# Kernel tuning notes

Measured on AMD Instinct MI355X. Metric: run time of the kernel, lower is better.

## Reference

```python
import jax, jax.numpy as jnp
import numpy as np

H = 768            # hidden_size
IMG_H = 1024       # image_hidden_size
NH = 12            # num_heads
NKV = 1            # num_kv_heads (MQA)
HD = H // NH       # head_dim = 64
FF = 4 * H         # intermediate_size = 3072
EPS = 1e-5


def layernorm(x, g, b):
    m = jnp.mean(x, axis=-1, keepdims=True)
    v = jnp.mean(jnp.square(x - m), axis=-1, keepdims=True)
    return (x - m) * jax.lax.rsqrt(v + EPS) * g + b


def setup_inputs() -> dict:
    key = jax.random.key(0)
    ks = jax.random.split(key, 12)
    B, NQ, NIMG = 8, 256, 4096
    s = 0.02
    return {
        "hidden_states": jax.random.normal(ks[0], (B, NQ, H), jnp.float32),
        "image_features": jax.random.normal(ks[1], (B, NIMG, IMG_H), jnp.float32),
        # norm_image_pre
        "ln_img_g": jnp.ones((IMG_H,), jnp.float32),
        "ln_img_b": jnp.zeros((IMG_H,), jnp.float32),
        # image_bottleneck (bias=False)
        "W_bottle": jax.random.normal(ks[2], (IMG_H, H), jnp.float32) * s,
        # norm_hidden
        "ln_h_g": jnp.ones((H,), jnp.float32),
        "ln_h_b": jnp.zeros((H,), jnp.float32),
        # to_q
        "Wq": jax.random.normal(ks[3], (H, H), jnp.float32) * s,
        "bq": jnp.zeros((H,), jnp.float32),
        # to_kv: out = num_kv_heads * head_dim * 2
        "Wkv": jax.random.normal(ks[4], (H, 2 * NKV * HD), jnp.float32) * s,
        "bkv": jnp.zeros((2 * NKV * HD,), jnp.float32),
        # to_out
        "Wo": jax.random.normal(ks[5], (H, H), jnp.float32) * s,
        "bo": jnp.zeros((H,), jnp.float32),
        # attn_out_norm
        "ln_ao_g": jnp.ones((H,), jnp.float32),
        "ln_ao_b": jnp.zeros((H,), jnp.float32),
        # gate
        "gate_param": jnp.zeros((), jnp.float32),
        # ffn_norm
        "ln_f_g": jnp.ones((H,), jnp.float32),
        "ln_f_b": jnp.zeros((H,), jnp.float32),
        # ffn
        "W1": jax.random.normal(ks[6], (H, FF), jnp.float32) * s,
        "b1": jnp.zeros((FF,), jnp.float32),
        "W2": jax.random.normal(ks[7], (FF, H), jnp.float32) * s,
        "b2": jnp.zeros((H,), jnp.float32),
    }


def reference(hidden_states, image_features, ln_img_g, ln_img_b, W_bottle,
              ln_h_g, ln_h_b, Wq, bq, Wkv, bkv, Wo, bo, ln_ao_g, ln_ao_b,
              gate_param, ln_f_g, ln_f_b, W1, b1, W2, b2):
    B, NQ, _ = hidden_states.shape
    # image pre-norm + bottleneck
    img = layernorm(image_features, ln_img_g, ln_img_b)
    img = img @ W_bottle                                   # [B, Nimg, H]
    # query path
    q_in = layernorm(hidden_states, ln_h_g, ln_h_b)
    q = (q_in @ Wq + bq).reshape(B, NQ, NH, HD).transpose(0, 2, 1, 3)  # b h i d
    # kv path (MQA: single shared KV head)
    kv = (img @ Wkv + bkv).reshape(B, -1, 2, NKV, HD)
    k = kv[:, :, 0, 0, :]                                  # [B, Nimg, HD]
    v = kv[:, :, 1, 0, :]
    scale = 1.0 / np.sqrt(HD)
    # broadcast KV across heads instead of explicit repeat
    scores = jnp.einsum('bhid,bjd->bhij', q * scale, k)    # [B, NH, NQ, Nimg]
    attn = jax.nn.softmax(scores, axis=-1)                 # dropout is identity (eval)
    out = jnp.einsum('bhij,bjd->bhid', attn, v)
    out = out.transpose(0, 2, 1, 3).reshape(B, NQ, H)
    out = out @ Wo + bo
    out = layernorm(out, ln_ao_g, ln_ao_b)
    gate = jax.nn.sigmoid(gate_param)
    h = hidden_states + gate * out
    ffn_in = layernorm(h, ln_f_g, ln_f_b)
    ffn_out = jax.nn.gelu(ffn_in @ W1 + b1, approximate=False) @ W2 + b2
    return h + ffn_out
```

## Files before the change

### kernel.cpp

```cpp
#include <hip/hip_runtime.h>
#include <cstdint>

typedef unsigned short u16;
typedef __bf16 bf16_t;
typedef bf16_t bf16x8 __attribute__((ext_vector_type(8)));
typedef float f32x4 __attribute__((ext_vector_type(4)));

__device__ __forceinline__ float b2f(u16 v) {
  union { uint32_t u; float f; } c; c.u = ((uint32_t)v) << 16; return c.f;
}
__device__ __forceinline__ u16 f2b(float f) {
  union { float f; uint32_t u; } c; c.f = f;
  uint32_t lsb = (c.u >> 16) & 1u;
  return (u16)((c.u + 0x7fffu + lsb) >> 16);
}
__device__ __forceinline__ uint4 pack8(f32x4 a, f32x4 b) {
  union { uint4 v; u16 s[8]; } r;
  r.s[0] = f2b(a[0]); r.s[1] = f2b(a[1]); r.s[2] = f2b(a[2]); r.s[3] = f2b(a[3]);
  r.s[4] = f2b(b[0]); r.s[5] = f2b(b[1]); r.s[6] = f2b(b[2]); r.s[7] = f2b(b[3]);
  return r.v;
}
__device__ __forceinline__ void phase_barrier() {
  asm volatile("s_waitcnt lgkmcnt(0)" ::: "memory");
  __builtin_amdgcn_s_barrier();
  asm volatile("" ::: "memory");
}
__device__ __forceinline__ void vm_drain() {
  asm volatile("s_waitcnt vmcnt(0)" ::: "memory");
}
__device__ __forceinline__ void gload_lds16(const u16* g, u16* l) {
  __builtin_amdgcn_global_load_lds((const __attribute__((address_space(1))) void*)g,
                                   (__attribute__((address_space(3))) void*)l, 16, 0, 0);
}
__device__ __forceinline__ int xcd_swizzle(int lid, int nwg) {
  int q = nwg >> 3, r = nwg & 7, x = lid & 7, s = lid >> 3;
  return (x < r ? x * (q + 1) : r * (q + 1) + (x - r) * q) + s;
}

__global__ __launch_bounds__(256) void transpose_f2b(const float* __restrict__ in,
                                                     u16* __restrict__ out, int R, int C) {
  __shared__ __align__(16) u16 tile[32][33];
  int tx = threadIdx.x & 31, ty = threadIdx.x >> 5;
  int c0 = blockIdx.x * 32, r0 = blockIdx.y * 32;
#pragma unroll
  for (int i = 0; i < 4; ++i) {
    int r = r0 + ty + i * 8, c = c0 + tx;
    if (r < R && c < C) tile[ty + i * 8][tx] = f2b(in[(size_t)r * C + c]);
  }
  __syncthreads();
#pragma unroll
  for (int i = 0; i < 4; ++i) {
    int oc = c0 + ty + i * 8, orr = r0 + tx;
    if (oc < C && orr < R) out[(size_t)oc * R + orr] = tile[tx][ty + i * 8];
  }
}

__global__ __launch_bounds__(256) void prep_wg(const u16* __restrict__ WT, const float* __restrict__ g,
                                               const float* __restrict__ b, u16* __restrict__ WgT,
                                               float* __restrict__ ucol, float* __restrict__ wcol,
                                               int K) {
  int n = blockIdx.x * 4 + (threadIdx.x >> 6);
  int lane = threadIdx.x & 63;
  const u16* src = WT + (size_t)n * K;
  u16* dst = WgT + (size_t)n * K;
  float su = 0.f, sw = 0.f;
  for (int k = lane; k < K; k += 64) {
    float wc = b2f(src[k]);
    float wg = g[k] * wc;
    dst[k] = f2b(wg);
    su += wg;
    sw += b[k] * wc;
  }
#pragma unroll
  for (int off = 32; off >= 1; off >>= 1) {
    su += __shfl_xor(su, off, 64);
    sw += __shfl_xor(sw, off, 64);
  }
  if (lane == 0) { ucol[n] = su; wcol[n] = sw; }
}

__global__ __launch_bounds__(256) void hs_prep(const float* __restrict__ hs, u16* __restrict__ out,
                                               float* __restrict__ rstdg, float* __restrict__ mrstdg) {
  int row = blockIdx.x * 4 + (threadIdx.x >> 6);
  int lane = threadIdx.x & 63;
  const float* x = hs + (size_t)row * 768;
  float v[12];
#pragma unroll
  for (int it = 0; it < 3; ++it) {
    int c = (lane + it * 64) * 4;
    f32x4 d = *(const f32x4*)(x + c);
    v[it * 4 + 0] = d[0]; v[it * 4 + 1] = d[1]; v[it * 4 + 2] = d[2]; v[it * 4 + 3] = d[3];
  }
  float s = 0.f, s2 = 0.f;
#pragma unroll
  for (int i = 0; i < 12; ++i) { s += v[i]; s2 += v[i] * v[i]; }
#pragma unroll
  for (int off = 32; off >= 1; off >>= 1) {
    s += __shfl_xor(s, off, 64);
    s2 += __shfl_xor(s2, off, 64);
  }
  float inv_n = 1.0f / 768.f;
  float mean = s * inv_n;
  float var = fmaxf(s2 * inv_n - mean * mean, 0.f);
  float rstd = rsqrtf(var + 1e-5f);
  if (lane == 0) { rstdg[row] = rstd; mrstdg[row] = mean * rstd; }
#pragma unroll
  for (int it = 0; it < 3; ++it) {
    int c = (lane + it * 64) * 4;
    uint2 po;
    po.x = (uint32_t)f2b(v[it * 4 + 0]) | ((uint32_t)f2b(v[it * 4 + 1]) << 16);
    po.y = (uint32_t)f2b(v[it * 4 + 2]) | ((uint32_t)f2b(v[it * 4 + 3]) << 16);
    *(uint2*)(out + (size_t)row * 768 + c) = po;
  }
}

__global__ __launch_bounds__(256) void ln_res(const u16* __restrict__ ao, const float* __restrict__ g,
                                              const float* __restrict__ bta,
                                              const float* __restrict__ hs,
                                              const float* __restrict__ gatep,
                                              float* __restrict__ hf, u16* __restrict__ hb,
                                              float* __restrict__ rstdg, float* __restrict__ mrstdg) {
  int row = blockIdx.x * 4 + (threadIdx.x >> 6);
  int lane = threadIdx.x & 63;
  const u16* xb = ao + (size_t)row * 768;
  float v[12];
#pragma unroll
  for (int it = 0; it < 3; ++it) {
    int c = (lane + it * 64) * 4;
    uint2 d = *(const uint2*)(xb + c);
    v[it * 4 + 0] = b2f(d.x & 0xffff); v[it * 4 + 1] = b2f(d.x >> 16);
    v[it * 4 + 2] = b2f(d.y & 0xffff); v[it * 4 + 3] = b2f(d.y >> 16);
  }
  float s = 0.f, s2 = 0.f;
#pragma unroll
  for (int i = 0; i < 12; ++i) { s += v[i]; s2 += v[i] * v[i]; }
#pragma unroll
  for (int off = 32; off >= 1; off >>= 1) {
    s += __shfl_xor(s, off, 64);
    s2 += __shfl_xor(s2, off, 64);
  }
  float inv_n = 1.0f / 768.f;
  float mean = s * inv_n;
  float var = fmaxf(s2 * inv_n - mean * mean, 0.f);
  float rstd = rsqrtf(var + 1e-5f);
  float gate = 1.f / (1.f + __expf(-gatep[0]));
  float hsum = 0.f, hsum2 = 0.f;
  float o[12];
#pragma unroll
  for (int it = 0; it < 3; ++it) {
    int c = (lane + it * 64) * 4;
    const float* rr = hs + (size_t)row * 768 + c;
#pragma unroll
    for (int i = 0; i < 4; ++i) {
      float hv = rr[i] + gate * ((v[it * 4 + i] - mean) * rstd * g[c + i] + bta[c + i]);
      o[it * 4 + i] = hv;
      hsum += hv; hsum2 += hv * hv;
    }
    *(f32x4*)(hf + (size_t)row * 768 + c) = (f32x4){o[it * 4 + 0], o[it * 4 + 1], o[it * 4 + 2], o[it * 4 + 3]};
    uint2 po;
    po.x = (uint32_t)f2b(o[it * 4 + 0]) | ((uint32_t)f2b(o[it * 4 + 1]) << 16);
    po.y = (uint32_t)f2b(o[it * 4 + 2]) | ((uint32_t)f2b(o[it * 4 + 3]) << 16);
    *(uint2*)(hb + (size_t)row * 768 + c) = po;
  }
#pragma unroll
  for (int off = 32; off >= 1; off >>= 1) {
    hsum += __shfl_xor(hsum, off, 64);
    hsum2 += __shfl_xor(hsum2, off, 64);
  }
  float hm = hsum * inv_n;
  float hvar = fmaxf(hsum2 * inv_n - hm * hm, 0.f);
  float hrstd = rsqrtf(hvar + 1e-5f);
  if (lane == 0) { rstdg[row] = hrstd; mrstdg[row] = hm * hrstd; }
}

template <int SPLITK, int AMODE, int BMODE, int EPI, bool OUTF32, bool VTOUT>
__device__ __forceinline__ void gemm_body(const void* __restrict__ Av, const void* __restrict__ Bv,
                                          const float* __restrict__ bias,
                                          const float* __restrict__ rstdg,
                                          const float* __restrict__ mrstdg,
                                          const float* __restrict__ ucol,
                                          const float* __restrict__ wcol,
                                          void* __restrict__ Cv, u16* __restrict__ VTout,
                                          int M, int N, int K) {
  __shared__ __align__(16) u16 aT[2][128 * 32];
  __shared__ __align__(16) u16 bT[2][128 * 32];
  __shared__ float rstd_s[EPI == 4 ? 128 : 1];
  __shared__ float mrstd_s[EPI == 4 ? 128 : 1];
  __shared__ __align__(16) u16 vtile[VTOUT ? 64 * 136 : 1];

  int gx = gridDim.x, gy = gridDim.y;
  int nwg = gx * gy * (int)gridDim.z;
  int lid = ((int)blockIdx.z * gy + (int)blockIdx.y) * gx + (int)blockIdx.x;
  int wid = xcd_swizzle(lid, nwg);
  int bz = wid / (gx * gy);
  int rem = wid - bz * (gx * gy);
  int bx = rem / gy;
  int by = rem - bx * gy;

  int t = threadIdx.x, lane = t & 63, wave = t >> 6;
  int quad = lane >> 4, lcol = lane & 15;
  int wm = (wave >> 1) * 64, wn = (wave & 1) * 64;
  const u16* Ab = (const u16*)Av;
  const float* Af = (const float*)Av;
  const u16* Bb = (const u16*)Bv;
  const float* Bf = (const float*)Bv;
  const int kchunk = (SPLITK > 1) ? K / SPLITK : K;
  const int kstart = (SPLITK > 1) ? bz * kchunk : 0;
  int rr = t >> 1, rc = t & 1;
  float sa = 0.f, sa2 = 0.f;
  f32x4 acc[4][4];
#pragma unroll
  for (int i = 0; i < 4; ++i)
#pragma unroll
    for (int j = 0; j < 4; ++j) acc[i][j] = (f32x4){0.f, 0.f, 0.f, 0.f};

  f32x4 araw[4], braw[4];

  auto dmaA = [&](int buf, int k0) {
#pragma unroll
    for (int s2 = 0; s2 < 2; ++s2) {
      int row = (wave * 2 + s2) * 16 + (lane >> 2);
      int ch = (lane & 3) ^ (row & 3);
      gload_lds16(Ab + (size_t)(bx * 128 + row) * K + kstart + k0 + ch * 8,
                  &aT[buf][(wave * 2 + s2) * 512]);
    }
  };
  auto dmaB = [&](int buf, int k0) {
#pragma unroll
    for (int s2 = 0; s2 < 2; ++s2) {
      int row = (wave * 2 + s2) * 16 + (lane >> 2);
      int ch = (lane & 3) ^ (row & 3);
      gload_lds16(Bb + (size_t)(by * 128 + row) * K + kstart + k0 + ch * 8,
                  &bT[buf][(wave * 2 + s2) * 512]);
    }
  };
  auto regloadA = [&](int k0) {
    const f32x4* p = (const f32x4*)&Af[(size_t)(bx * 128 + rr) * K + kstart + k0 + rc * 16];
#pragma unroll
    for (int i = 0; i < 4; ++i) araw[i] = p[i];
  };
  auto regstoreA = [&](int buf) {
    if (EPI == 4) {
#pragma unroll
      for (int i = 0; i < 4; ++i)
#pragma unroll
        for (int j = 0; j < 4; ++j) { sa += araw[i][j]; sa2 += araw[i][j] * araw[i][j]; }
    }
    uint4 c0 = pack8(araw[0], araw[1]), c1 = pack8(araw[2], araw[3]);
    *(uint4*)&aT[buf][rr * 32 + (((rc * 2 + 0) ^ (rr & 3)) << 3)] = c0;
    *(uint4*)&aT[buf][rr * 32 + (((rc * 2 + 1) ^ (rr & 3)) << 3)] = c1;
  };
  auto regloadB = [&](int k0) {
    const f32x4* p = (const f32x4*)&Bf[(size_t)(by * 128 + rr) * K + kstart + k0 + rc * 16];
#pragma unroll
    for (int i = 0; i < 4; ++i) braw[i] = p[i];
  };
  auto regstoreB = [&](int buf) {
    uint4 c0 = pack8(braw[0], braw[1]), c1 = pack8(braw[2], braw[3]);
    *(uint4*)&bT[buf][rr * 32 + (((rc * 2 + 0) ^ (rr & 3)) << 3)] = c0;
    *(uint4*)&bT[buf][rr * 32 + (((rc * 2 + 1) ^ (rr & 3)) << 3)] = c1;
  };
  auto stage_load = [&](int buf, int k0) {
    if (AMODE == 1) regloadA(k0); else dmaA(buf, k0);
    if (BMODE == 1) regloadB(k0); else dmaB(buf, k0);
  };
  auto stage_store = [&](int buf) {
    if (AMODE == 1) regstoreA(buf);
    if (BMODE == 1) regstoreB(buf);
  };
  auto compute = [&](int buf) {
    bf16x8 af[4], bfr[4];
#pragma unroll
    for (int mt = 0; mt < 4; ++mt) {
      int r = wm + mt * 16 + lcol;
      af[mt] = *(const bf16x8*)&aT[buf][r * 32 + (((quad ^ (r & 3))) << 3)];
    }
#pragma unroll
    for (int nt = 0; nt < 4; ++nt) {
      int r = wn + nt * 16 + lcol;
      bfr[nt] = *(const bf16x8*)&bT[buf][r * 32 + (((quad ^ (r & 3))) << 3)];
    }
#pragma unroll
    for (int mt = 0; mt < 4; ++mt)
#pragma unroll
      for (int nt = 0; nt < 4; ++nt)
        acc[mt][nt] = __builtin_amdgcn_mfma_f32_16x16x32_bf16(af[mt], bfr[nt], acc[mt][nt], 0, 0, 0);
  };

  const int nk = kchunk >> 5;
  stage_load(0, 0);
  stage_store(0);
  vm_drain();
  phase_barrier();
  int cur = 0;
  for (int kt = 0; kt < nk; ++kt) {
    bool more = kt + 1 < nk;
    if (more) stage_load(cur ^ 1, (kt + 1) << 5);
    compute(cur);
    if (more) stage_store(cur ^ 1);
    vm_drain();
    phase_barrier();
    cur ^= 1;
  }

  if (EPI == 4) {
    float s = sa, s2 = sa2;
    s += __shfl_xor(s, 1, 64);
    s2 += __shfl_xor(s2, 1, 64);
    if ((t & 1) == 0) {
      float inv_n = 1.0f / (float)K;
      float mean = s * inv_n;
      float var = fmaxf(s2 * inv_n - mean * mean, 0.f);
      float rstd = rsqrtf(var + 1e-5f);
      rstd_s[rr] = rstd;
      mrstd_s[rr] = mean * rstd;
    }
    __syncthreads();
  }

  if (VTOUT) {
    u16* kb = (u16*)Cv;
#pragma unroll
    for (int mt = 0; mt < 4; ++mt) {
#pragma unroll
      for (int nt = 0; nt < 4; ++nt) {
#pragma unroll
        for (int r = 0; r < 4; ++r) {
          int lrow = wm + mt * 16 + quad * 4 + r;
          int row = bx * 128 + lrow;
          int col = wn + nt * 16 + lcol;
          float v = rstd_s[lrow] * acc[mt][nt][r] - mrstd_s[lrow] * ucol[col] + wcol[col] + bias[col];
          u16 hv = f2b(v);
          if (wn == 0) kb[(size_t)row * 64 + col] = hv;
          else vtile[(col - 64) * 136 + lrow] = hv;
        }
      }
    }
    __syncthreads();
    int dd = t >> 2, js = (t & 3) * 32;
    int bg = bx >> 5, j0g = (bx & 31) * 128;
    u16* dst = VTout + ((size_t)bg * 64 + dd) * 4096 + j0g + js;
#pragma unroll
    for (int i = 0; i < 4; ++i)
      *(uint4*)(dst + i * 8) = *(const uint4*)&vtile[dd * 136 + js + i * 8];
    return;
  }

  u16* Cb = (u16*)Cv;
  float* Cf = (float*)Cv;
  if (SPLITK > 1) Cf += (size_t)bz * (size_t)M * (size_t)N;
#pragma unroll
  for (int mt = 0; mt < 4; ++mt) {
#pragma unroll
    for (int nt = 0; nt < 4; ++nt) {
#pragma unroll
      for (int r = 0; r < 4; ++r) {
        int lrow = wm + mt * 16 + quad * 4 + r;
        int row = bx * 128 + lrow;
        int col = by * 128 + wn + nt * 16 + lcol;
        float v = acc[mt][nt][r];
        if (EPI == 1) v += bias[col];
        if (EPI == 3 || EPI == 5)
          v = rstdg[row] * v - mrstdg[row] * ucol[col] + wcol[col] + bias[col];
        if (EPI == 5) v = 0.5f * v * (1.f + erff(v * 0.70710678118f));
        size_t idx = (size_t)row * N + col;
        if (OUTF32) Cf[idx] = v; else Cb[idx] = f2b(v);
      }
    }
  }
}

#define GEMM_ARGS const void* Av, const void* Bv, const float* bias, const float* rstdg, \
                  const float* mrstdg, const float* ucol, const float* wcol, void* Cv,   \
                  u16* VTout, int M, int N, int K
__global__ __launch_bounds__(256) void gemm_wc(GEMM_ARGS) {
  gemm_body<1, 0, 1, 0, false, false>(Av, Bv, bias, rstdg, mrstdg, ucol, wcol, Cv, VTout, M, N, K);
}
__global__ __launch_bounds__(256) void gemm_kv(GEMM_ARGS) {
  gemm_body<1, 1, 0, 4, false, true>(Av, Bv, bias, rstdg, mrstdg, ucol, wcol, Cv, VTout, M, N, K);
}
__global__ __launch_bounds__(256) void gemm_q(GEMM_ARGS) {
  gemm_body<1, 0, 0, 3, false, false>(Av, Bv, bias, rstdg, mrstdg, ucol, wcol, Cv, VTout, M, N, K);
}
__global__ __launch_bounds__(256) void gemm_o(GEMM_ARGS) {
  gemm_body<1, 0, 0, 1, false, false>(Av, Bv, bias, rstdg, mrstdg, ucol, wcol, Cv, VTout, M, N, K);
}
__global__ __launch_bounds__(256) void gemm_w1(GEMM_ARGS) {
  gemm_body<1, 0, 0, 5, false, false>(Av, Bv, bias, rstdg, mrstdg, ucol, wcol, Cv, VTout, M, N, K);
}
__global__ __launch_bounds__(256) void gemm_w2(GEMM_ARGS) {
  gemm_body<2, 0, 0, 0, true, false>(Av, Bv, bias, rstdg, mrstdg, ucol, wcol, Cv, VTout, M, N, K);
}

__global__ __launch_bounds__(256) void w2_merge(const float* __restrict__ part,
                                                const float* __restrict__ hf,
                                                const float* __restrict__ b2,
                                                float* __restrict__ out) {
  int idx = blockIdx.x * 256 + threadIdx.x;
  f32x4 p0 = ((const f32x4*)part)[idx];
  f32x4 p1 = ((const f32x4*)part)[idx + 393216];
  f32x4 h = ((const f32x4*)hf)[idx];
  f32x4 bb = ((const f32x4*)b2)[idx % 192];
  f32x4 o;
#pragma unroll
  for (int i = 0; i < 4; ++i) o[i] = p0[i] + p1[i] + h[i] + bb[i];
  ((f32x4*)out)[idx] = o;
}

__global__ __launch_bounds__(256) void attn_kernel(const u16* __restrict__ qbuf,
                                                   const u16* __restrict__ kb,
                                                   const u16* __restrict__ VT,
                                                   float* __restrict__ Opart,
                                                   float* __restrict__ lpart) {
  __shared__ __align__(16) u16 k_lds[64 * 72];
  __shared__ __align__(16) u16 vt_lds[64 * 72];
  __shared__ __align__(16) u16 p_lds[4 * 16 * 72];
  int lid = ((int)blockIdx.z * 12 + (int)blockIdx.y) * 4 + (int)blockIdx.x;
  int wid = (lid & 7) * 96 + (lid >> 3);
  int bi = wid & 3;
  int h = (wid >> 2) % 12;
  int z = wid / 48;
  int b = z >> 1, s = z & 1;
  int t = threadIdx.x;
  int wave = t >> 6, lane = t & 63, quad = lane >> 4, lcol = lane & 15;
  int i0 = bi * 64 + wave * 16;
  const u16* qrow = qbuf + ((size_t)(b * 256 + i0 + lcol) * 768 + h * 64 + quad * 8);
  bf16x8 qf0 = *(const bf16x8*)qrow;
  bf16x8 qf1 = *(const bf16x8*)(qrow + 32);
  float l_r[4] = {0.f, 0.f, 0.f, 0.f};
  f32x4 oacc[4];
#pragma unroll
  for (int nt = 0; nt < 4; ++nt) oacc[nt] = (f32x4){0.f, 0.f, 0.f, 0.f};
  int sr = t >> 2, sc = (t & 3) * 16;
  const u16* kbase = kb + (size_t)b * 4096 * 64;
  const u16* vtbase = VT + (size_t)b * 64 * 4096;
  u16* pw = &p_lds[wave * 16 * 72];

  for (int jt = 0; jt < 32; ++jt) {
    int j0 = s * 2048 + jt * 64;
    const u16* krow = kbase + (size_t)(j0 + sr) * 64 + sc;
    *(uint4*)&k_lds[sr * 72 + sc] = *(const uint4*)(krow);
    *(uint4*)&k_lds[sr * 72 + sc + 8] = *(const uint4*)(krow + 8);
    const u16* vrow = vtbase + (size_t)sr * 4096 + j0 + sc;
    *(uint4*)&vt_lds[sr * 72 + sc] = *(const uint4*)(vrow);
    *(uint4*)&vt_lds[sr * 72 + sc + 8] = *(const uint4*)(vrow + 8);
    __syncthreads();

    f32x4 sc4[4];
#pragma unroll
    for (int nt = 0; nt < 4; ++nt) sc4[nt] = (f32x4){0.f, 0.f, 0.f, 0.f};
#pragma unroll
    for (int nt = 0; nt < 4; ++nt) {
      bf16x8 kb0 = *(const bf16x8*)&k_lds[(nt * 16 + lcol) * 72 + quad * 8];
      bf16x8 kb1 = *(const bf16x8*)&k_lds[(nt * 16 + lcol) * 72 + 32 + quad * 8];
      sc4[nt] = __builtin_amdgcn_mfma_f32_16x16x32_bf16(qf0, kb0, sc4[nt], 0, 0, 0);
      sc4[nt] = __builtin_amdgcn_mfma_f32_16x16x32_bf16(qf1, kb1, sc4[nt], 0, 0, 0);
    }
#pragma unroll
    for (int r = 0; r < 4; ++r) {
      float rsum = 0.f;
#pragma unroll
      for (int nt = 0; nt < 4; ++nt) {
        float p = __expf(sc4[nt][r] * 0.125f);
        sc4[nt][r] = p;
        rsum += p;
      }
      rsum += __shfl_xor(rsum, 1, 64);
      rsum += __shfl_xor(rsum, 2, 64);
      rsum += __shfl_xor(rsum, 4, 64);
      rsum += __shfl_xor(rsum, 8, 64);
      l_r[r] += rsum;
#pragma unroll
      for (int nt = 0; nt < 4; ++nt) pw[(quad * 4 + r) * 72 + nt * 16 + lcol] = f2b(sc4[nt][r]);
    }
#pragma unroll
    for (int ks = 0; ks < 2; ++ks) {
      bf16x8 pa = *(const bf16x8*)&pw[lcol * 72 + ks * 32 + quad * 8];
#pragma unroll
      for (int nt = 0; nt < 4; ++nt) {
        bf16x8 vb = *(const bf16x8*)&vt_lds[(nt * 16 + lcol) * 72 + ks * 32 + quad * 8];
        oacc[nt] = __builtin_amdgcn_mfma_f32_16x16x32_bf16(pa, vb, oacc[nt], 0, 0, 0);
      }
    }
    __syncthreads();
  }
  size_t base = ((size_t)z * 12 + h) * 256;
#pragma unroll
  for (int r = 0; r < 4; ++r) {
    int row = bi * 64 + wave * 16 + quad * 4 + r;
#pragma unroll
    for (int nt = 0; nt < 4; ++nt)
      Opart[(base + row) * 64 + nt * 16 + lcol] = oacc[nt][r];
    if (lcol == 0) lpart[base + row] = l_r[r];
  }
}

__global__ __launch_bounds__(256) void attn_merge(const float* __restrict__ Opart,
                                                  const float* __restrict__ lpart,
                                                  u16* __restrict__ attn_o) {
  int row = blockIdx.x;
  int col = blockIdx.y * 256 + threadIdx.x;
  int b = row >> 8, i = row & 255, h = col >> 6, d = col & 63;
  size_t i0 = (((size_t)(b * 2 + 0) * 12 + h) * 256 + i);
  size_t i1 = (((size_t)(b * 2 + 1) * 12 + h) * 256 + i);
  float o = Opart[i0 * 64 + d] + Opart[i1 * 64 + d];
  float l = lpart[i0] + lpart[i1];
  attn_o[(size_t)row * 768 + col] = f2b(o / l);
}

extern "C" void kernel_launch(void* const* d_in, const int* in_sizes, int n_in, void* d_out,
                              int out_size, void* d_ws, size_t ws_size, hipStream_t stream) {
  (void)in_sizes; (void)n_in; (void)out_size; (void)ws_size;
  const float* hs = (const float*)d_in[0];
  const float* imgf = (const float*)d_in[1];
  const float* ln_img_g = (const float*)d_in[2];
  const float* ln_img_b = (const float*)d_in[3];
  const float* W_bottle = (const float*)d_in[4];
  const float* ln_h_g = (const float*)d_in[5];
  const float* ln_h_b = (const float*)d_in[6];
  const float* Wq = (const float*)d_in[7];
  const float* bq = (const float*)d_in[8];
  const float* Wkv = (const float*)d_in[9];
  const float* bkv = (const float*)d_in[10];
  const float* Wo = (const float*)d_in[11];
  const float* bo = (const float*)d_in[12];
  const float* ln_ao_g = (const float*)d_in[13];
  const float* ln_ao_b = (const float*)d_in[14];
  const float* gatep = (const float*)d_in[15];
  const float* ln_f_g = (const float*)d_in[16];
  const float* ln_f_b = (const float*)d_in[17];
  const float* W1 = (const float*)d_in[18];
  const float* b1 = (const float*)d_in[19];
  const float* W2 = (const float*)d_in[20];
  const float* b2 = (const float*)d_in[21];

  char* sc = (char*)d_ws;
  auto alloc = [&](size_t bytes) {
    char* p = sc;
    sc += (bytes + 63) & ~(size_t)63;
    return p;
  };
  u16* WTq = (u16*)alloc(768 * 768 * 2);
  u16* WTo = (u16*)alloc(768 * 768 * 2);
  u16* WT1 = (u16*)alloc(3072 * 768 * 2);
  u16* WT2 = (u16*)alloc(768 * 3072 * 2);
  u16* WkvT = (u16*)alloc(128 * 768 * 2);
  u16* WcT = (u16*)alloc(128 * 1024 * 2);
  u16* WgT = (u16*)alloc(128 * 1024 * 2);
  u16* WqgT = (u16*)alloc(768 * 768 * 2);
  u16* W1gT = (u16*)alloc(3072 * 768 * 2);
  float* ucol = (float*)alloc(128 * 4);
  float* wcol = (float*)alloc(128 * 4);
  float* uq = (float*)alloc(768 * 4);
  float* wq = (float*)alloc(768 * 4);
  float* u1 = (float*)alloc(3072 * 4);
  float* w1c = (float*)alloc(3072 * 4);
  float* rstdq = (float*)alloc(2048 * 4);
  float* mrstdq = (float*)alloc(2048 * 4);
  float* rstdh = (float*)alloc(2048 * 4);
  float* mrstdh = (float*)alloc(2048 * 4);
  u16* hs16 = (u16*)alloc(2048 * 768 * 2);
  u16* kb = (u16*)alloc((size_t)32768 * 64 * 2);
  u16* VT = (u16*)alloc((size_t)8 * 64 * 4096 * 2);
  u16* qb = (u16*)alloc(2048 * 768 * 2);
  u16* attn_o = (u16*)alloc(2048 * 768 * 2);
  u16* ao = (u16*)alloc(2048 * 768 * 2);
  u16* hbuf = (u16*)alloc(2048 * 768 * 2);
  float* hf32 = (float*)alloc(2048 * 768 * 4);
  u16* actb = (u16*)alloc((size_t)2048 * 3072 * 2);
  float* Opart = (float*)alloc((size_t)16 * 12 * 256 * 64 * 4);
  float* lpart = (float*)alloc((size_t)16 * 12 * 256 * 4);

  transpose_f2b<<<dim3(24, 24), 256, 0, stream>>>(Wq, WTq, 768, 768);
  transpose_f2b<<<dim3(24, 24), 256, 0, stream>>>(Wo, WTo, 768, 768);
  transpose_f2b<<<dim3(96, 24), 256, 0, stream>>>(W1, WT1, 768, 3072);
  transpose_f2b<<<dim3(24, 96), 256, 0, stream>>>(W2, WT2, 3072, 768);
  transpose_f2b<<<dim3(4, 24), 256, 0, stream>>>(Wkv, WkvT, 768, 128);

  gemm_wc<<<dim3(1, 8), 256, 0, stream>>>(WkvT, W_bottle, nullptr, nullptr, nullptr, nullptr,
                                          nullptr, WcT, nullptr, 128, 1024, 768);
  prep_wg<<<32, 256, 0, stream>>>(WcT, ln_img_g, ln_img_b, WgT, ucol, wcol, 1024);
  prep_wg<<<192, 256, 0, stream>>>(WTq, ln_h_g, ln_h_b, WqgT, uq, wq, 768);
  prep_wg<<<768, 256, 0, stream>>>(WT1, ln_f_g, ln_f_b, W1gT, u1, w1c, 768);
  hs_prep<<<512, 256, 0, stream>>>(hs, hs16, rstdq, mrstdq);
  gemm_kv<<<dim3(256, 1), 256, 0, stream>>>(imgf, WgT, bkv, nullptr, nullptr, ucol, wcol,
                                            kb, VT, 32768, 128, 1024);
  gemm_q<<<dim3(16, 6), 256, 0, stream>>>(hs16, WqgT, bq, rstdq, mrstdq, uq, wq,
                                          qb, nullptr, 2048, 768, 768);
  attn_kernel<<<dim3(4, 12, 16), 256, 0, stream>>>(qb, kb, VT, Opart, lpart);
  attn_merge<<<dim3(2048, 3), 256, 0, stream>>>(Opart, lpart, attn_o);
  gemm_o<<<dim3(16, 6), 256, 0, stream>>>(attn_o, WTo, bo, nullptr, nullptr, nullptr, nullptr,
                                          ao, nullptr, 2048, 768, 768);
  ln_res<<<512, 256, 0, stream>>>(ao, ln_ao_g, ln_ao_b, hs, gatep, hf32, hbuf, rstdh, mrstdh);
  gemm_w1<<<dim3(16, 24), 256, 0, stream>>>(hbuf, W1gT, b1, rstdh, mrstdh, u1, w1c,
                                            actb, nullptr, 2048, 3072, 768);
  gemm_w2<<<dim3(16, 6, 2), 256, 0, stream>>>(actb, WT2, nullptr, nullptr, nullptr, nullptr, nullptr,
                                              Opart, nullptr, 2048, 768, 3072);
  w2_merge<<<1536, 256, 0, stream>>>(Opart, hf32, b2, (float*)d_out);
}
```

Before: 536.0 us.

## Double-buffer attention K/V tiles, templatize GEMM tile height, smaller tiles for narrow GEMMs

Attention K/V loads are now double-buffered: the next tile is fetched into registers during compute and stored to the alternate LDS buffer, which removes one barrier per iteration. The P conversion uses packed v_cvt_pk_bf16_f32, and MFMA sections are wrapped in s_setprio to favour the matrix work. The GEMM body takes a BM template parameter, so the q, o and w2 GEMMs run with 64-row tiles and twice as many workgroups to fill more CUs. The trade-offs are more LDS in attention and lower per-block reuse in the smaller GEMM tiles.

New measurement: 519.1 us. 1.03x faster.

```diff
diff --git a/kernel.cpp b/kernel.cpp
--- a/kernel.cpp
+++ b/kernel.cpp
@@ -19,6 +19,11 @@
   r.s[0] = f2b(a[0]); r.s[1] = f2b(a[1]); r.s[2] = f2b(a[2]); r.s[3] = f2b(a[3]);
   r.s[4] = f2b(b[0]); r.s[5] = f2b(b[1]); r.s[6] = f2b(b[2]); r.s[7] = f2b(b[3]);
   return r.v;
+}
+__device__ __forceinline__ uint32_t cvt_pk_bf16(float lo, float hi) {
+  uint32_t r;
+  asm("v_cvt_pk_bf16_f32 %0, %1, %2" : "=v"(r) : "v"(lo), "v"(hi));
+  return r;
 }
 __device__ __forceinline__ void phase_barrier() {
   asm volatile("s_waitcnt lgkmcnt(0)" ::: "memory");
@@ -173,7 +178,7 @@
   if (lane == 0) { rstdg[row] = hrstd; mrstdg[row] = hm * hrstd; }
 }
 
-template <int SPLITK, int AMODE, int BMODE, int EPI, bool OUTF32, bool VTOUT>
+template <int BM, int SPLITK, int AMODE, int BMODE, int EPI, bool OUTF32, bool VTOUT>
 __device__ __forceinline__ void gemm_body(const void* __restrict__ Av, const void* __restrict__ Bv,
                                           const float* __restrict__ bias,
                                           const float* __restrict__ rstdg,
@@ -182,7 +187,9 @@
                                           const float* __restrict__ wcol,
                                           void* __restrict__ Cv, u16* __restrict__ VTout,
                                           int M, int N, int K) {
-  __shared__ __align__(16) u16 aT[2][128 * 32];
+  constexpr int MT = BM / 32;
+  constexpr int AL = BM / 64;
+  __shared__ __align__(16) u16 aT[2][BM * 32];
   __shared__ __align__(16) u16 bT[2][128 * 32];
   __shared__ float rstd_s[EPI == 4 ? 128 : 1];
   __shared__ float mrstd_s[EPI == 4 ? 128 : 1];
@@ -199,7 +206,7 @@
 
   int t = threadIdx.x, lane = t & 63, wave = t >> 6;
   int quad = lane >> 4, lcol = lane & 15;
-  int wm = (wave >> 1) * 64, wn = (wave & 1) * 64;
+  int wm = (wave >> 1) * (16 * MT), wn = (wave & 1) * 64;
   const u16* Ab = (const u16*)Av;
   const float* Af = (const float*)Av;
   const u16* Bb = (const u16*)Bv;
@@ -208,9 +215,9 @@
   const int kstart = (SPLITK > 1) ? bz * kchunk : 0;
   int rr = t >> 1, rc = t & 1;
   float sa = 0.f, sa2 = 0.f;
-  f32x4 acc[4][4];
-#pragma unroll
-  for (int i = 0; i < 4; ++i)
+  f32x4 acc[MT][4];
+#pragma unroll
+  for (int i = 0; i < MT; ++i)
 #pragma unroll
     for (int j = 0; j < 4; ++j) acc[i][j] = (f32x4){0.f, 0.f, 0.f, 0.f};
 
@@ -218,11 +225,11 @@
 
   auto dmaA = [&](int buf, int k0) {
 #pragma unroll
-    for (int s2 = 0; s2 < 2; ++s2) {
-      int row = (wave * 2 + s2) * 16 + (lane >> 2);
+    for (int s2 = 0; s2 < AL; ++s2) {
+      int row = (wave * AL + s2) * 16 + (lane >> 2);
       int ch = (lane & 3) ^ (row & 3);
-      gload_lds16(Ab + (size_t)(bx * 128 + row) * K + kstart + k0 + ch * 8,
-                  &aT[buf][(wave * 2 + s2) * 512]);
+      gload_lds16(Ab + (size_t)(bx * BM + row) * K + kstart + k0 + ch * 8,
+                  &aT[buf][(wave * AL + s2) * 512]);
     }
   };
   auto dmaB = [&](int buf, int k0) {
@@ -235,7 +242,7 @@
     }
   };
   auto regloadA = [&](int k0) {
-    const f32x4* p = (const f32x4*)&Af[(size_t)(bx * 128 + rr) * K + kstart + k0 + rc * 16];
+    const f32x4* p = (const f32x4*)&Af[(size_t)(bx * BM + rr) * K + kstart + k0 + rc * 16];
 #pragma unroll
     for (int i = 0; i < 4; ++i) araw[i] = p[i];
   };
@@ -269,9 +276,9 @@
     if (BMODE == 1) regstoreB(buf);
   };
   auto compute = [&](int buf) {
-    bf16x8 af[4], bfr[4];
-#pragma unroll
-    for (int mt = 0; mt < 4; ++mt) {
+    bf16x8 af[MT], bfr[4];
+#pragma unroll
+    for (int mt = 0; mt < MT; ++mt) {
       int r = wm + mt * 16 + lcol;
       af[mt] = *(const bf16x8*)&aT[buf][r * 32 + (((quad ^ (r & 3))) << 3)];
     }
@@ -281,7 +288,7 @@
       bfr[nt] = *(const bf16x8*)&bT[buf][r * 32 + (((quad ^ (r & 3))) << 3)];
     }
 #pragma unroll
-    for (int mt = 0; mt < 4; ++mt)
+    for (int mt = 0; mt < MT; ++mt)
 #pragma unroll
       for (int nt = 0; nt < 4; ++nt)
         acc[mt][nt] = __builtin_amdgcn_mfma_f32_16x16x32_bf16(af[mt], bfr[nt], acc[mt][nt], 0, 0, 0);
@@ -321,13 +328,13 @@
   if (VTOUT) {
     u16* kb = (u16*)Cv;
 #pragma unroll
-    for (int mt = 0; mt < 4; ++mt) {
+    for (int mt = 0; mt < MT; ++mt) {
 #pragma unroll
       for (int nt = 0; nt < 4; ++nt) {
 #pragma unroll
         for (int r = 0; r < 4; ++r) {
           int lrow = wm + mt * 16 + quad * 4 + r;
-          int row = bx * 128 + lrow;
+          int row = bx * BM + lrow;
           int col = wn + nt * 16 + lcol;
           float v = rstd_s[lrow] * acc[mt][nt][r] - mrstd_s[lrow] * ucol[col] + wcol[col] + bias[col];
           u16 hv = f2b(v);
@@ -350,13 +357,13 @@
   float* Cf = (float*)Cv;
   if (SPLITK > 1) Cf += (size_t)bz * (size_t)M * (size_t)N;
 #pragma unroll
-  for (int mt = 0; mt < 4; ++mt) {
+  for (int mt = 0; mt < MT; ++mt) {
 #pragma unroll
     for (int nt = 0; nt < 4; ++nt) {
 #pragma unroll
       for (int r = 0; r < 4; ++r) {
         int lrow = wm + mt * 16 + quad * 4 + r;
-        int row = bx * 128 + lrow;
+        int row = bx * BM + lrow;
         int col = by * 128 + wn + nt * 16 + lcol;
         float v = acc[mt][nt][r];
         if (EPI == 1) v += bias[col];
@@ -374,22 +381,22 @@
                   const float* mrstdg, const float* ucol, const float* wcol, void* Cv,   \
                   u16* VTout, int M, int N, int K
 __global__ __launch_bounds__(256) void gemm_wc(GEMM_ARGS) {
-  gemm_body<1, 0, 1, 0, false, false>(Av, Bv, bias, rstdg, mrstdg, ucol, wcol, Cv, VTout, M, N, K);
+  gemm_body<128, 1, 0, 1, 0, false, false>(Av, Bv, bias, rstdg, mrstdg, ucol, wcol, Cv, VTout, M, N, K);
 }
 __global__ __launch_bounds__(256) void gemm_kv(GEMM_ARGS) {
-  gemm_body<1, 1, 0, 4, false, true>(Av, Bv, bias, rstdg, mrstdg, ucol, wcol, Cv, VTout, M, N, K);
+  gemm_body<128, 1, 1, 0, 4, false, true>(Av, Bv, bias, rstdg, mrstdg, ucol, wcol, Cv, VTout, M, N, K);
 }
 __global__ __launch_bounds__(256) void gemm_q(GEMM_ARGS) {
-  gemm_body<1, 0, 0, 3, false, false>(Av, Bv, bias, rstdg, mrstdg, ucol, wcol, Cv, VTout, M, N, K);
+  gemm_body<64, 1, 0, 0, 3, false, false>(Av, Bv, bias, rstdg, mrstdg, ucol, wcol, Cv, VTout, M, N, K);
 }
 __global__ __launch_bounds__(256) void gemm_o(GEMM_ARGS) {
-  gemm_body<1, 0, 0, 1, false, false>(Av, Bv, bias, rstdg, mrstdg, ucol, wcol, Cv, VTout, M, N, K);
+  gemm_body<64, 1, 0, 0, 1, false, false>(Av, Bv, bias, rstdg, mrstdg, ucol, wcol, Cv, VTout, M, N, K);
 }
 __global__ __launch_bounds__(256) void gemm_w1(GEMM_ARGS) {
-  gemm_body<1, 0, 0, 5, false, false>(Av, Bv, bias, rstdg, mrstdg, ucol, wcol, Cv, VTout, M, N, K);
+  gemm_body<128, 1, 0, 0, 5, false, false>(Av, Bv, bias, rstdg, mrstdg, ucol, wcol, Cv, VTout, M, N, K);
 }
 __global__ __launch_bounds__(256) void gemm_w2(GEMM_ARGS) {
-  gemm_body<2, 0, 0, 0, true, false>(Av, Bv, bias, rstdg, mrstdg, ucol, wcol, Cv, VTout, M, N, K);
+  gemm_body<64, 2, 0, 0, 0, true, false>(Av, Bv, bias, rstdg, mrstdg, ucol, wcol, Cv, VTout, M, N, K);
 }
 
 __global__ __launch_bounds__(256) void w2_merge(const float* __restrict__ part,
@@ -412,8 +419,8 @@
                                                    const u16* __restrict__ VT,
                                                    float* __restrict__ Opart,
                                                    float* __restrict__ lpart) {
-  __shared__ __align__(16) u16 k_lds[64 * 72];
-  __shared__ __align__(16) u16 vt_lds[64 * 72];
+  __shared__ __align__(16) u16 k_lds[2][64 * 72];
+  __shared__ __align__(16) u16 vt_lds[2][64 * 72];
   __shared__ __align__(16) u16 p_lds[4 * 16 * 72];
   int lid = ((int)blockIdx.z * 12 + (int)blockIdx.y) * 4 + (int)blockIdx.x;
   int wid = (lid & 7) * 96 + (lid >> 3);
@@ -436,26 +443,43 @@
   const u16* vtbase = VT + (size_t)b * 64 * 4096;
   u16* pw = &p_lds[wave * 16 * 72];
 
-  for (int jt = 0; jt < 32; ++jt) {
+  uint4 kr0, kr1, vr0, vr1;
+  auto stage_load = [&](int jt) {
     int j0 = s * 2048 + jt * 64;
     const u16* krow = kbase + (size_t)(j0 + sr) * 64 + sc;
-    *(uint4*)&k_lds[sr * 72 + sc] = *(const uint4*)(krow);
-    *(uint4*)&k_lds[sr * 72 + sc + 8] = *(const uint4*)(krow + 8);
+    kr0 = *(const uint4*)(krow);
+    kr1 = *(const uint4*)(krow + 8);
     const u16* vrow = vtbase + (size_t)sr * 4096 + j0 + sc;
-    *(uint4*)&vt_lds[sr * 72 + sc] = *(const uint4*)(vrow);
-    *(uint4*)&vt_lds[sr * 72 + sc + 8] = *(const uint4*)(vrow + 8);
-    __syncthreads();
+    vr0 = *(const uint4*)(vrow);
+    vr1 = *(const uint4*)(vrow + 8);
+  };
+  auto stage_store = [&](int buf) {
+    *(uint4*)&k_lds[buf][sr * 72 + sc] = kr0;
+    *(uint4*)&k_lds[buf][sr * 72 + sc + 8] = kr1;
+    *(uint4*)&vt_lds[buf][sr * 72 + sc] = vr0;
+    *(uint4*)&vt_lds[buf][sr * 72 + sc + 8] = vr1;
+  };
+
+  stage_load(0);
+  stage_store(0);
+  phase_barrier();
+  int cur = 0;
+  for (int jt = 0; jt < 32; ++jt) {
+    bool more = jt + 1 < 32;
+    if (more) stage_load(jt + 1);
 
     f32x4 sc4[4];
 #pragma unroll
     for (int nt = 0; nt < 4; ++nt) sc4[nt] = (f32x4){0.f, 0.f, 0.f, 0.f};
+    __builtin_amdgcn_s_setprio(1);
 #pragma unroll
     for (int nt = 0; nt < 4; ++nt) {
-      bf16x8 kb0 = *(const bf16x8*)&k_lds[(nt * 16 + lcol) * 72 + quad * 8];
-      bf16x8 kb1 = *(const bf16x8*)&k_lds[(nt * 16 + lcol) * 72 + 32 + quad * 8];
+      bf16x8 kb0 = *(const bf16x8*)&k_lds[cur][(nt * 16 + lcol) * 72 + quad * 8];
+      bf16x8 kb1 = *(const bf16x8*)&k_lds[cur][(nt * 16 + lcol) * 72 + 32 + quad * 8];
       sc4[nt] = __builtin_amdgcn_mfma_f32_16x16x32_bf16(qf0, kb0, sc4[nt], 0, 0, 0);
       sc4[nt] = __builtin_amdgcn_mfma_f32_16x16x32_bf16(qf1, kb1, sc4[nt], 0, 0, 0);
     }
+    __builtin_amdgcn_s_setprio(0);
 #pragma unroll
     for (int r = 0; r < 4; ++r) {
       float rsum = 0.f;
@@ -470,19 +494,28 @@
       rsum += __shfl_xor(rsum, 4, 64);
       rsum += __shfl_xor(rsum, 8, 64);
       l_r[r] += rsum;
-#pragma unroll
-      for (int nt = 0; nt < 4; ++nt) pw[(quad * 4 + r) * 72 + nt * 16 + lcol] = f2b(sc4[nt][r]);
-    }
+      uint32_t pk01 = cvt_pk_bf16(sc4[0][r], sc4[1][r]);
+      uint32_t pk23 = cvt_pk_bf16(sc4[2][r], sc4[3][r]);
+      int prow = (quad * 4 + r) * 72 + lcol;
+      pw[prow] = (u16)(pk01 & 0xffff);
+      pw[prow + 16] = (u16)(pk01 >> 16);
+      pw[prow + 32] = (u16)(pk23 & 0xffff);
+      pw[prow + 48] = (u16)(pk23 >> 16);
+    }
+    __builtin_amdgcn_s_setprio(1);
 #pragma unroll
     for (int ks = 0; ks < 2; ++ks) {
       bf16x8 pa = *(const bf16x8*)&pw[lcol * 72 + ks * 32 + quad * 8];
 #pragma unroll
       for (int nt = 0; nt < 4; ++nt) {
-        bf16x8 vb = *(const bf16x8*)&vt_lds[(nt * 16 + lcol) * 72 + ks * 32 + quad * 8];
+        bf16x8 vb = *(const bf16x8*)&vt_lds[cur][(nt * 16 + lcol) * 72 + ks * 32 + quad * 8];
         oacc[nt] = __builtin_amdgcn_mfma_f32_16x16x32_bf16(pa, vb, oacc[nt], 0, 0, 0);
       }
     }
-    __syncthreads();
+    __builtin_amdgcn_s_setprio(0);
+    if (more) stage_store(cur ^ 1);
+    phase_barrier();
+    cur ^= 1;
   }
   size_t base = ((size_t)z * 12 + h) * 256;
 #pragma unroll
@@ -585,16 +618,16 @@
   hs_prep<<<512, 256, 0, stream>>>(hs, hs16, rstdq, mrstdq);
   gemm_kv<<<dim3(256, 1), 256, 0, stream>>>(imgf, WgT, bkv, nullptr, nullptr, ucol, wcol,
                                             kb, VT, 32768, 128, 1024);
-  gemm_q<<<dim3(16, 6), 256, 0, stream>>>(hs16, WqgT, bq, rstdq, mrstdq, uq, wq,
+  gemm_q<<<dim3(32, 6), 256, 0, stream>>>(hs16, WqgT, bq, rstdq, mrstdq, uq, wq,
                                           qb, nullptr, 2048, 768, 768);
   attn_kernel<<<dim3(4, 12, 16), 256, 0, stream>>>(qb, kb, VT, Opart, lpart);
   attn_merge<<<dim3(2048, 3), 256, 0, stream>>>(Opart, lpart, attn_o);
-  gemm_o<<<dim3(16, 6), 256, 0, stream>>>(attn_o, WTo, bo, nullptr, nullptr, nullptr, nullptr,
+  gemm_o<<<dim3(32, 6), 256, 0, stream>>>(attn_o, WTo, bo, nullptr, nullptr, nullptr, nullptr,
                                           ao, nullptr, 2048, 768, 768);
   ln_res<<<512, 256, 0, stream>>>(ao, ln_ao_g, ln_ao_b, hs, gatep, hf32, hbuf, rstdh, mrstdh);
   gemm_w1<<<dim3(16, 24), 256, 0, stream>>>(hbuf, W1gT, b1, rstdh, mrstdh, u1, w1c,
                                             actb, nullptr, 2048, 3072, 768);
-  gemm_w2<<<dim3(16, 6, 2), 256, 0, stream>>>(actb, WT2, nullptr, nullptr, nullptr, nullptr, nullptr,
+  gemm_w2<<<dim3(32, 6, 2), 256, 0, stream>>>(actb, WT2, nullptr, nullptr, nullptr, nullptr, nullptr,
                                               Opart, nullptr, 2048, 768, 3072);
   w2_merge<<<1536, 256, 0, stream>>>(Opart, hf32, b2, (float*)d_out);
 }
```
